# Optimization experiments

Measured on AMD Instinct MI355X. Metric: run time of the kernel, lower is better.

The kernel has to match this reference:

```python
import jax, jax.numpy as jnp
import numpy as np

B, DIM, H, W = 8, 256, 128, 128
P = 4               # patch_size
HEADS = 8
HD = DIM // HEADS   # head dim = 32
CPB_HIDDEN = 512    # hidden width of the dynamic RPE MLP


def setup_inputs() -> dict:
    key = jax.random.key(0)
    ks = jax.random.split(key, 12)
    s = 0.02
    return {
        "x": jax.random.normal(ks[0], (B, DIM, H, W), dtype=jnp.float32),
        # PatchEmbed2d: Conv2d(dim, dim, kernel=P, stride=P)  weight [O, I, P, P]
        "w_embed": jax.random.normal(ks[1], (DIM, DIM, P, P), dtype=jnp.float32) * s,
        "b_embed": jnp.zeros((DIM,), dtype=jnp.float32),
        # DynamicPosEncoder: MLP(2 -> CPB_HIDDEN -> HEADS) on relative coords
        "cpb_w1": jax.random.normal(ks[2], (CPB_HIDDEN, 2), dtype=jnp.float32) * s,
        "cpb_b1": jnp.zeros((CPB_HIDDEN,), dtype=jnp.float32),
        "cpb_w2": jax.random.normal(ks[3], (HEADS, CPB_HIDDEN), dtype=jnp.float32) * s,
        # MaskAttention2d
        "w_qkv": jax.random.normal(ks[4], (3 * DIM, DIM), dtype=jnp.float32) * s,
        "b_qkv": jnp.zeros((3 * DIM,), dtype=jnp.float32),
        "w_proj": jax.random.normal(ks[5], (DIM, DIM), dtype=jnp.float32) * s,
        "b_proj": jnp.zeros((DIM,), dtype=jnp.float32),
        # PatchUnEmbed2d: ConvTranspose2d(dim, dim, kernel=P, stride=P)  weight [I, O, P, P]
        "w_unembed": jax.random.normal(ks[6], (DIM, DIM, P, P), dtype=jnp.float32) * s,
        "b_unembed": jnp.zeros((DIM,), dtype=jnp.float32),
    }


def _rpe_bias(Hp, Wp, cpb_w1, cpb_b1, cpb_w2):
    """Dynamic relative position bias -> [HEADS, N, N], N = Hp*Wp."""
    # continuous relative-coordinate table [(2Hp-1)*(2Wp-1), 2], normalized to [-1, 1]
    rh = (jnp.arange(2 * Hp - 1, dtype=jnp.float32) - (Hp - 1)) / max(Hp - 1, 1)
    rw = (jnp.arange(2 * Wp - 1, dtype=jnp.float32) - (Wp - 1)) / max(Wp - 1, 1)
    rel = jnp.stack(jnp.meshgrid(rh, rw, indexing="ij"), axis=-1).reshape(-1, 2)
    table = jax.nn.relu(rel @ cpb_w1.T + cpb_b1) @ cpb_w2.T  # [(2Hp-1)(2Wp-1), HEADS]
    # static relative position index [N, N]
    ch = np.arange(Hp)
    cw = np.arange(Wp)
    coords = np.stack(np.meshgrid(ch, cw, indexing="ij")).reshape(2, -1)  # [2, N]
    d = coords[:, :, None] - coords[:, None, :]                           # [2, N, N]
    idx = (d[0] + Hp - 1) * (2 * Wp - 1) + (d[1] + Wp - 1)               # [N, N]
    bias = table[jnp.asarray(idx)]                                        # [N, N, HEADS]
    return bias.transpose(2, 0, 1)                                        # [HEADS, N, N]


def reference(x, w_embed, b_embed, cpb_w1, cpb_b1, cpb_w2,
              w_qkv, b_qkv, w_proj, b_proj, w_unembed, b_unembed):
    Bx, C, Hf, Wf = x.shape
    Hp, Wp = Hf // P, Wf // P
    N = Hp * Wp
    # ---- patch embed: Conv2d(k=P, s=P) as block reshape + einsum ----
    xr = x.reshape(Bx, C, Hp, P, Wp, P)
    z = jnp.einsum("bchpwq,ocpq->bohw", xr, w_embed) + b_embed[None, :, None, None]
    # ---- dynamic RPE bias ----
    bias = _rpe_bias(Hp, Wp, cpb_w1, cpb_b1, cpb_w2)  # [HEADS, N, N]
    # ---- multi-head self-attention over the Hp*Wp grid ----
    tok = z.reshape(Bx, C, N).transpose(0, 2, 1)                     # [B, N, C]
    qkv = tok @ w_qkv.T + b_qkv                                       # [B, N, 3C]
    qkv = qkv.reshape(Bx, N, 3, HEADS, HD).transpose(2, 0, 3, 1, 4)   # [3, B, H, N, hd]
    q, k, v = qkv[0], qkv[1], qkv[2]
    scale = HD ** -0.5
    attn = jnp.einsum("bhnd,bhmd->bhnm", q * scale, k) + bias[None]   # [B, H, N, N]
    attn = jax.nn.softmax(attn, axis=-1)
    out = jnp.einsum("bhnm,bhmd->bhnd", attn, v)                      # [B, H, N, hd]
    out = out.transpose(0, 2, 1, 3).reshape(Bx, N, C)
    out = out @ w_proj.T + b_proj                                     # [B, N, C]
    z2 = out.transpose(0, 2, 1).reshape(Bx, C, Hp, Wp)
    # ---- patch unembed: ConvTranspose2d(k=P, s=P) as einsum + block reshape ----
    y = jnp.einsum("bchw,copq->bohpwq", z2, w_unembed)
    y = y.reshape(Bx, C, Hf, Wf) + b_unembed[None, :, None, None]
    return y
```

## Files before the change

### kernel.cpp

```cpp
#include <hip/hip_runtime.h>
#include <cstdint>
#include <cstddef>


typedef __bf16 bf16x8 __attribute__((ext_vector_type(8)));
typedef float f32x4 __attribute__((ext_vector_type(4)));
typedef unsigned short u16x4 __attribute__((ext_vector_type(4)));

__device__ __forceinline__ unsigned short f2bf(float f) {
  unsigned u = __builtin_bit_cast(unsigned, f);
  u += 0x7fffu + ((u >> 16) & 1u);
  return (unsigned short)(u >> 16);
}
__device__ __forceinline__ float bf2f(unsigned short u) {
  return __builtin_bit_cast(float, ((unsigned)u) << 16);
}

__device__ __forceinline__ void async_ld16(const void* g, void* l) {
  __builtin_amdgcn_global_load_lds(
      (const __attribute__((address_space(1))) void*)g,
      (__attribute__((address_space(3))) void*)l, 16, 0, 0);
}

__global__ __launch_bounds__(256) void rpe_table_kernel(
    const float* __restrict__ w1, const float* __restrict__ b1,
    const float* __restrict__ w2, float* __restrict__ table) {
  int t = blockIdx.x * 256 + threadIdx.x;
  if (t >= 3969) return;
  int a = t / 63, c = t - a * 63;
  float rh = (float)(a - 31) * (1.0f / 31.0f);
  float rw = (float)(c - 31) * (1.0f / 31.0f);
  float acc[8];
#pragma unroll
  for (int h = 0; h < 8; h++) acc[h] = 0.f;
  for (int j = 0; j < 512; j++) {
    float hv = fmaxf(rh * w1[2 * j] + rw * w1[2 * j + 1] + b1[j], 0.f);
#pragma unroll
    for (int h = 0; h < 8; h++) acc[h] += hv * w2[h * 512 + j];
  }
#pragma unroll
  for (int h = 0; h < 8; h++) table[t * 8 + h] = acc[h];
}

__global__ __launch_bounds__(256) void bias_expand_kernel(
    const float* __restrict__ table, unsigned short* __restrict__ biasQK) {
  int t = blockIdx.x * 256 + threadIdx.x;
  int k8 = t & 127;
  int q = (t >> 7) & 1023;
  int h = t >> 17;
  int k0 = k8 * 8;
  int qh = q >> 5, qw = q & 31;
  int kh = k0 >> 5, kw0 = k0 & 31;
  int idxbase = (qh - kh + 31) * 63 + (qw - kw0 + 31);
  unsigned short pk[8];
#pragma unroll
  for (int j = 0; j < 8; j++)
    pk[j] = f2bf(table[(size_t)(idxbase - j) * 8 + h]);
  *(uint4*)(biasQK + ((size_t)h << 20) + (size_t)q * 1024 + k0) =
      *(const uint4*)pk;
}

__global__ __launch_bounds__(256) void cvt_bf16_kernel(
    const float* __restrict__ src, unsigned short* __restrict__ dst, int n8) {
  int i = blockIdx.x * 256 + threadIdx.x;
  if (i >= n8) return;
  const float4* s4 = (const float4*)src + (size_t)i * 2;
  float4 a = s4[0], b = s4[1];
  unsigned short t[8] = {f2bf(a.x), f2bf(a.y), f2bf(a.z), f2bf(a.w),
                         f2bf(b.x), f2bf(b.y), f2bf(b.z), f2bf(b.w)};
  *(uint4*)(dst + (size_t)i * 8) = *(const uint4*)t;
}

__global__ __launch_bounds__(256) void transpose_cvt_kernel(
    const float* __restrict__ src, unsigned short* __restrict__ dst) {
  __shared__ float tile[32][33];
  int bx = blockIdx.x;
  int by = blockIdx.y;
  int tx = threadIdx.x & 31, ty = threadIdx.x >> 5;
#pragma unroll
  for (int r = 0; r < 32; r += 8)
    tile[ty + r][tx] = src[(size_t)(by * 32 + ty + r) * 4096 + bx * 32 + tx];
  __syncthreads();
#pragma unroll
  for (int r = 0; r < 32; r += 8)
    dst[(size_t)(bx * 32 + ty + r) * 256 + by * 32 + tx] = f2bf(tile[tx][ty + r]);
}

__global__ __launch_bounds__(256) void im2col_bf16_kernel(
    const float* __restrict__ x, unsigned short* __restrict__ A) {
  int gid = blockIdx.x * 256 + threadIdx.x;
  int bn = gid & 8191;
  int c = gid >> 13;
  int b = bn >> 10;
  int hw = bn & 1023;
  int h = hw >> 5, w = hw & 31;
  const float4* x4 = (const float4*)x;
  int base = ((b * 256 + c) * 128 + 4 * h) * 32 + w;
  unsigned short t[16];
#pragma unroll
  for (int p = 0; p < 4; p++) {
    float4 v = x4[base + p * 32];
    t[p * 4 + 0] = f2bf(v.x); t[p * 4 + 1] = f2bf(v.y);
    t[p * 4 + 2] = f2bf(v.z); t[p * 4 + 3] = f2bf(v.w);
  }
  unsigned short* dst = A + (size_t)bn * 4096 + c * 16;
  *(uint4*)dst = *(const uint4*)t;
  *(uint4*)(dst + 8) = *(const uint4*)(t + 8);
}

__global__ __launch_bounds__(256) void splitk_reduce_kernel(
    const float* __restrict__ part, const float* __restrict__ bias,
    unsigned short* __restrict__ out) {
  size_t i = ((size_t)blockIdx.x * 256 + threadIdx.x) * 8;
  const float4* p = (const float4*)(part + i);
  const size_t s4 = 2097152 / 4;
  float4 a0 = p[0], a1 = p[1];
#pragma unroll
  for (int s = 1; s < 4; s++) {
    float4 b0 = p[s * s4], b1 = p[s * s4 + 1];
    a0.x += b0.x; a0.y += b0.y; a0.z += b0.z; a0.w += b0.w;
    a1.x += b1.x; a1.y += b1.y; a1.z += b1.z; a1.w += b1.w;
  }
  int col = (int)(i & 255);
  unsigned short t8[8] = {
      f2bf(a0.x + bias[col + 0]), f2bf(a0.y + bias[col + 1]),
      f2bf(a0.z + bias[col + 2]), f2bf(a0.w + bias[col + 3]),
      f2bf(a1.x + bias[col + 4]), f2bf(a1.y + bias[col + 5]),
      f2bf(a1.z + bias[col + 6]), f2bf(a1.w + bias[col + 7])};
  *(uint4*)(out + i) = *(const uint4*)t8;
}

template <int CMODE>
__global__ __launch_bounds__(256) void gemm_mfma_kernel(
    const unsigned short* __restrict__ A, const unsigned short* __restrict__ B,
    const float* __restrict__ bias, void* __restrict__ Cv,
    int M, int N, int K, int lda, int ldb, int ldc) {
  __shared__ unsigned short As[2 * 128 * 32];
  __shared__ unsigned short Bs[2 * 128 * 32];
  int tid = threadIdx.x;
  int lane = tid & 63;
  int wave = tid >> 6;
  int m0 = blockIdx.y * 128, n0 = blockIdx.x * 128;
  int wm = (wave & 1) * 64, wn = (wave >> 1) * 64;

  if (CMODE == 4) {
    int s = blockIdx.z;
    A += (size_t)s * K;
    B += (size_t)s * K;
    Cv = (void*)((float*)Cv + (size_t)s * M * N);
  }

  f32x4 acc[4][4];
#pragma unroll
  for (int i = 0; i < 4; i++)
#pragma unroll
    for (int j = 0; j < 4; j++) acc[i][j] = (f32x4){0.f, 0.f, 0.f, 0.f};

  int f0 = tid, f1 = tid + 256;
  const unsigned short* Ag0 = A + (size_t)(m0 + (f0 >> 2)) * lda + (f0 & 3) * 8;
  const unsigned short* Ag1 = A + (size_t)(m0 + (f1 >> 2)) * lda + (f1 & 3) * 8;
  const unsigned short* Bg0 = B + (size_t)(n0 + (f0 >> 2)) * ldb + (f0 & 3) * 8;
  const unsigned short* Bg1 = B + (size_t)(n0 + (f1 >> 2)) * ldb + (f1 & 3) * 8;
  unsigned short* Al0 = As + f0 * 8;
  unsigned short* Al1 = As + f1 * 8;
  unsigned short* Bl0 = Bs + f0 * 8;
  unsigned short* Bl1 = Bs + f1 * 8;

  int fr = lane & 15;
  int fh = lane >> 4;

  int ntiles = K >> 5;
  async_ld16(Ag0, Al0);
  async_ld16(Ag1, Al1);
  async_ld16(Bg0, Bl0);
  async_ld16(Bg1, Bl1);
  __syncthreads();

  for (int t = 0; t < ntiles; t++) {
    int cur = (t & 1) << 12;
    int nxt = cur ^ 4096;
    if (t + 1 < ntiles) {
      int kn = (t + 1) << 5;
      async_ld16(Ag0 + kn, Al0 + nxt);
      async_ld16(Ag1 + kn, Al1 + nxt);
      async_ld16(Bg0 + kn, Bl0 + nxt);
      async_ld16(Bg1 + kn, Bl1 + nxt);
    }
    const unsigned short* Asc = As + cur;
    const unsigned short* Bsc = Bs + cur;
    bf16x8 af[4], bfr[4];
#pragma unroll
    for (int tt = 0; tt < 4; tt++) {
      af[tt] = *(const bf16x8*)(Asc + (wm + tt * 16 + fr) * 32 + fh * 8);
      bfr[tt] = *(const bf16x8*)(Bsc + (wn + tt * 16 + fr) * 32 + fh * 8);
    }
#pragma unroll
    for (int mt = 0; mt < 4; mt++)
#pragma unroll
      for (int nt = 0; nt < 4; nt++)
        acc[mt][nt] = __builtin_amdgcn_mfma_f32_16x16x32_bf16(
            af[mt], bfr[nt], acc[mt][nt], 0, 0, 0);
    __syncthreads();
  }

#pragma unroll
  for (int mt = 0; mt < 4; mt++) {
    int row0 = m0 + wm + mt * 16 + fh * 4;
    if (CMODE == 2) {
      int b = row0 >> 10, hp = (row0 >> 5) & 31, wp = row0 & 31;
      size_t rowoff0 = (size_t)b * 4194304 + hp * 512 + wp * 4;
      float* y = (float*)Cv;
#pragma unroll
      for (int nt = 0; nt < 4; nt++) {
        int col = n0 + wn + nt * 16 + fr;
        int o = col >> 4, p = (col >> 2) & 3, q = col & 3;
        size_t coloff = (size_t)o * 16384 + p * 128 + q;
        float bv = bias[o];
#pragma unroll
        for (int r = 0; r < 4; r++)
          y[rowoff0 + r * 4 + coloff] = acc[mt][nt][r] + bv;
      }
    } else if (CMODE == 3) {
      unsigned short* base = (unsigned short*)Cv;
#pragma unroll
      for (int nt = 0; nt < 4; nt++) {
        int col = n0 + wn + nt * 16 + fr;
        int which = col >> 8, hh = (col >> 5) & 7, d = col & 31;
        float bv = bias[col];
#pragma unroll
        for (int r = 0; r < 4; r++) {
          int row = row0 + r;
          int bb = row >> 10, nn = row & 1023;
          int bh = bb * 8 + hh;
          float v = acc[mt][nt][r] + bv;
          if (which == 0) v *= 0.17677669529663687f;
          size_t addr;
          if (which < 2)
            addr = (size_t)which * 2097152 + ((size_t)bh * 1024 + nn) * 32 + d;
          else
            addr = (size_t)2 * 2097152 + (size_t)bh * 32768 + (size_t)d * 1024 + nn;
          base[addr] = f2bf(v);
        }
      }
    } else if (CMODE == 4) {
      float* Cp = (float*)Cv;
#pragma unroll
      for (int nt = 0; nt < 4; nt++) {
        int col = n0 + wn + nt * 16 + fr;
#pragma unroll
        for (int r = 0; r < 4; r++)
          Cp[(size_t)(row0 + r) * ldc + col] = acc[mt][nt][r];
      }
    } else {
#pragma unroll
      for (int nt = 0; nt < 4; nt++) {
        int col = n0 + wn + nt * 16 + fr;
        float bv = bias ? bias[col] : 0.f;
        unsigned short* C = (unsigned short*)Cv;
#pragma unroll
        for (int r = 0; r < 4; r++)
          C[(size_t)(row0 + r) * ldc + col] = f2bf(acc[mt][nt][r] + bv);
      }
    }
  }
}

__global__ __launch_bounds__(256) void attn_mfma_kernel(
    const unsigned short* __restrict__ Qb, const unsigned short* __restrict__ Kb,
    const unsigned short* __restrict__ Vtb,
    const unsigned short* __restrict__ biasQK,
    unsigned short* __restrict__ out) {
  __shared__ unsigned short sm[21888];
  unsigned short* Ks = sm;
  unsigned short* Vt = sm + 2304;
  unsigned short* Bsh = sm + 4480;
  unsigned short* Qs = sm + 13184;
  unsigned short* Ps = sm + 13184;

  int tid = threadIdx.x;
  int lane = tid & 63, w = tid >> 6;
  int n = lane & 15, g = lane >> 4;
  int blk = blockIdx.x;
  int qt = blk & 7, b = (blk >> 3) & 7, h = blk >> 6;
  int bh = b * 8 + h;
  int q0 = qt * 128;

  const unsigned short* Qg = Qb + ((size_t)bh * 1024 + q0) * 32;
  const unsigned short* Kg = Kb + (size_t)bh * 1024 * 32;
  const unsigned short* Vg = Vtb + (size_t)bh * 32 * 1024;
  const unsigned short* Bg = biasQK + ((size_t)h << 20) + (size_t)q0 * 1024;

#pragma unroll
  for (int i = 0; i < 2; i++) {
    int idx = i * 256 + tid;
    int r = idx >> 2, c = idx & 3;
    *(uint4*)(Qs + r * 36 + c * 8) = *(const uint4*)(Qg + (size_t)r * 32 + c * 8);
  }
  __syncthreads();
  bf16x8 qf[2];
  qf[0] = *(const bf16x8*)(Qs + (w * 32 + n) * 36 + g * 8);
  qf[1] = *(const bf16x8*)(Qs + (w * 32 + 16 + n) * 36 + g * 8);

  f32x4 oacc[2][2];
#pragma unroll
  for (int i = 0; i < 2; i++)
#pragma unroll
    for (int j = 0; j < 2; j++) oacc[i][j] = (f32x4){0.f, 0.f, 0.f, 0.f};
  float m_run[2] = {-1e30f, -1e30f}, l_run[2] = {0.f, 0.f};

  unsigned short* Pw = Ps + w * 2176;

  for (int ks = 0; ks < 16; ks++) {
    int k0 = ks * 64;
    __syncthreads();
    {
      int r = tid >> 2, c = tid & 3;
      *(uint4*)(Ks + r * 36 + c * 8) =
          *(const uint4*)(Kg + (size_t)(k0 + r) * 32 + c * 8);
    }
    {
      int d = tid >> 3, c = tid & 7;
      *(uint4*)(Vt + d * 68 + c * 8) =
          *(const uint4*)(Vg + (size_t)d * 1024 + k0 + c * 8);
    }
#pragma unroll
    for (int i = 0; i < 4; i++) {
      int idx = i * 256 + tid;
      int r = idx >> 3, c = idx & 7;
      *(uint4*)(Bsh + r * 68 + c * 8) =
          *(const uint4*)(Bg + (size_t)r * 1024 + k0 + c * 8);
    }
    __syncthreads();

    bf16x8 kf[4];
#pragma unroll
    for (int mt = 0; mt < 4; mt++)
      kf[mt] = *(const bf16x8*)(Ks + (mt * 16 + n) * 36 + g * 8);
    f32x4 s[4][2];
#pragma unroll
    for (int mt = 0; mt < 4; mt++)
#pragma unroll
      for (int nt = 0; nt < 2; nt++)
        s[mt][nt] = __builtin_amdgcn_mfma_f32_16x16x32_bf16(
            kf[mt], qf[nt], (f32x4){0.f, 0.f, 0.f, 0.f}, 0, 0, 0);

#pragma unroll
    for (int mt = 0; mt < 4; mt++)
#pragma unroll
      for (int nt = 0; nt < 2; nt++) {
        u16x4 bb = *(const u16x4*)(Bsh + (w * 32 + nt * 16 + n) * 68 +
                                   mt * 16 + g * 4);
#pragma unroll
        for (int r = 0; r < 4; r++) s[mt][nt][r] += bf2f(bb[r]);
      }

    float alpha[2];
#pragma unroll
    for (int nt = 0; nt < 2; nt++) {
      float mx = -1e30f;
#pragma unroll
      for (int mt = 0; mt < 4; mt++)
#pragma unroll
        for (int r = 0; r < 4; r++) mx = fmaxf(mx, s[mt][nt][r]);
      mx = fmaxf(mx, __shfl_xor(mx, 16, 64));
      mx = fmaxf(mx, __shfl_xor(mx, 32, 64));
      float m_new = fmaxf(m_run[nt], mx);
      alpha[nt] = __expf(m_run[nt] - m_new);
      m_run[nt] = m_new;
      float ls = 0.f;
#pragma unroll
      for (int mt = 0; mt < 4; mt++) {
#pragma unroll
        for (int r = 0; r < 4; r++) {
          float p = __expf(s[mt][nt][r] - m_new);
          s[mt][nt][r] = p;
          ls += p;
        }
        u16x4 pk = {f2bf(s[mt][nt][0]), f2bf(s[mt][nt][1]),
                    f2bf(s[mt][nt][2]), f2bf(s[mt][nt][3])};
        *(u16x4*)(Pw + (nt * 16 + n) * 68 + mt * 16 + g * 4) = pk;
      }
      ls += __shfl_xor(ls, 16, 64);
      ls += __shfl_xor(ls, 32, 64);
      l_run[nt] = l_run[nt] * alpha[nt] + ls;
    }

#pragma unroll
    for (int dt = 0; dt < 2; dt++)
#pragma unroll
      for (int nt = 0; nt < 2; nt++)
#pragma unroll
        for (int r = 0; r < 4; r++) oacc[dt][nt][r] *= alpha[nt];
#pragma unroll
    for (int kt = 0; kt < 2; kt++) {
      bf16x8 vf[2], pf[2];
#pragma unroll
      for (int dt = 0; dt < 2; dt++)
        vf[dt] = *(const bf16x8*)(Vt + (dt * 16 + n) * 68 + kt * 32 + g * 8);
#pragma unroll
      for (int nt = 0; nt < 2; nt++)
        pf[nt] = *(const bf16x8*)(Pw + (nt * 16 + n) * 68 + kt * 32 + g * 8);
#pragma unroll
      for (int dt = 0; dt < 2; dt++)
#pragma unroll
        for (int nt = 0; nt < 2; nt++)
          oacc[dt][nt] = __builtin_amdgcn_mfma_f32_16x16x32_bf16(
              vf[dt], pf[nt], oacc[dt][nt], 0, 0, 0);
    }
  }

  float inv[2] = {1.f / l_run[0], 1.f / l_run[1]};
#pragma unroll
  for (int dt = 0; dt < 2; dt++)
#pragma unroll
    for (int nt = 0; nt < 2; nt++)
#pragma unroll
      for (int r = 0; r < 4; r++) {
        int d = dt * 16 + g * 4 + r;
        int q = q0 + w * 32 + nt * 16 + n;
        out[(size_t)(b * 1024 + q) * 256 + h * 32 + d] =
            f2bf(oacc[dt][nt][r] * inv[nt]);
      }
}

extern "C" void kernel_launch(void* const* d_in, const int* in_sizes, int n_in,
                              void* d_out, int out_size, void* d_ws, size_t ws_size,
                              hipStream_t stream) {
  const float* x         = (const float*)d_in[0];
  const float* w_embed   = (const float*)d_in[1];
  const float* b_embed   = (const float*)d_in[2];
  const float* cpb_w1    = (const float*)d_in[3];
  const float* cpb_b1    = (const float*)d_in[4];
  const float* cpb_w2    = (const float*)d_in[5];
  const float* w_qkv     = (const float*)d_in[6];
  const float* b_qkv     = (const float*)d_in[7];
  const float* w_proj    = (const float*)d_in[8];
  const float* b_proj    = (const float*)d_in[9];
  const float* w_unembed = (const float*)d_in[10];
  const float* b_unembed = (const float*)d_in[11];
  float* out = (float*)d_out;

  char* w = (char*)d_ws;
  unsigned short* Abig  = (unsigned short*)w; w += (size_t)8192 * 4096 * 2;
  unsigned short* tok   = (unsigned short*)w; w += (size_t)8192 * 256 * 2;
  unsigned short* qkvB  = (unsigned short*)w; w += (size_t)3 * 2097152 * 2;
  unsigned short* attno = (unsigned short*)w; w += (size_t)8192 * 256 * 2;
  unsigned short* z2    = (unsigned short*)w; w += (size_t)8192 * 256 * 2;
  float*          table = (float*)w;          w += (size_t)32768 * 4;
  unsigned short* biasQ = (unsigned short*)w; w += (size_t)8388608 * 2;
  unsigned short* wE    = (unsigned short*)w; w += (size_t)1048576 * 2;
  unsigned short* wQ    = (unsigned short*)w; w += (size_t)196608 * 2;
  unsigned short* wP    = (unsigned short*)w; w += (size_t)65536 * 2;
  unsigned short* wUt   = (unsigned short*)w; w += (size_t)1048576 * 2;

  unsigned short* Qb  = qkvB;
  unsigned short* Kb  = qkvB + 2097152;
  unsigned short* Vtb = qkvB + 2 * 2097152;

  float* Cpart = (float*)qkvB;

  cvt_bf16_kernel<<<512, 256, 0, stream>>>(w_embed, wE, 131072);
  cvt_bf16_kernel<<<96, 256, 0, stream>>>(w_qkv, wQ, 24576);
  cvt_bf16_kernel<<<32, 256, 0, stream>>>(w_proj, wP, 8192);
  transpose_cvt_kernel<<<dim3(128, 8), 256, 0, stream>>>(w_unembed, wUt);
  im2col_bf16_kernel<<<8192, 256, 0, stream>>>(x, Abig);

  gemm_mfma_kernel<4><<<dim3(2, 64, 4), 256, 0, stream>>>(
      Abig, wE, nullptr, Cpart, 8192, 256, 1024, 4096, 4096, 256);
  splitk_reduce_kernel<<<1024, 256, 0, stream>>>(Cpart, b_embed, tok);

  rpe_table_kernel<<<16, 256, 0, stream>>>(cpb_w1, cpb_b1, cpb_w2, table);
  bias_expand_kernel<<<4096, 256, 0, stream>>>(table, biasQ);

  gemm_mfma_kernel<3><<<dim3(6, 64), 256, 0, stream>>>(
      tok, wQ, b_qkv, qkvB, 8192, 768, 256, 256, 256, 0);
  attn_mfma_kernel<<<512, 256, 0, stream>>>(Qb, Kb, Vtb, biasQ, attno);
  gemm_mfma_kernel<1><<<dim3(2, 64), 256, 0, stream>>>(
      attno, wP, b_proj, z2, 8192, 256, 256, 256, 256, 256);
  gemm_mfma_kernel<2><<<dim3(32, 64), 256, 0, stream>>>(
      z2, wUt, b_unembed, out, 8192, 4096, 256, 256, 256, 0);
}
```

Measured before the change: 562.0 us.

## Compute RPE bias on the fly from LDS table, double-buffer K/V in attention

```diff
diff --git a/kernel.cpp b/kernel.cpp
--- a/kernel.cpp
+++ b/kernel.cpp
@@ -24,7 +24,7 @@
 
 __global__ __launch_bounds__(256) void rpe_table_kernel(
     const float* __restrict__ w1, const float* __restrict__ b1,
-    const float* __restrict__ w2, float* __restrict__ table) {
+    const float* __restrict__ w2, float* __restrict__ tableT) {
   int t = blockIdx.x * 256 + threadIdx.x;
   if (t >= 3969) return;
   int a = t / 63, c = t - a * 63;
@@ -39,25 +39,7 @@
     for (int h = 0; h < 8; h++) acc[h] += hv * w2[h * 512 + j];
   }
 #pragma unroll
-  for (int h = 0; h < 8; h++) table[t * 8 + h] = acc[h];
-}
-
-__global__ __launch_bounds__(256) void bias_expand_kernel(
-    const float* __restrict__ table, unsigned short* __restrict__ biasQK) {
-  int t = blockIdx.x * 256 + threadIdx.x;
-  int k8 = t & 127;
-  int q = (t >> 7) & 1023;
-  int h = t >> 17;
-  int k0 = k8 * 8;
-  int qh = q >> 5, qw = q & 31;
-  int kh = k0 >> 5, kw0 = k0 & 31;
-  int idxbase = (qh - kh + 31) * 63 + (qw - kw0 + 31);
-  unsigned short pk[8];
-#pragma unroll
-  for (int j = 0; j < 8; j++)
-    pk[j] = f2bf(table[(size_t)(idxbase - j) * 8 + h]);
-  *(uint4*)(biasQK + ((size_t)h << 20) + (size_t)q * 1024 + k0) =
-      *(const uint4*)pk;
+  for (int h = 0; h < 8; h++) tableT[h * 4096 + t] = acc[h];
 }
 
 __global__ __launch_bounds__(256) void cvt_bf16_kernel(
@@ -265,17 +247,17 @@
   }
 }
 
-__global__ __launch_bounds__(256) void attn_mfma_kernel(
+__global__ __launch_bounds__(512) void attn_mfma_kernel(
     const unsigned short* __restrict__ Qb, const unsigned short* __restrict__ Kb,
     const unsigned short* __restrict__ Vtb,
-    const unsigned short* __restrict__ biasQK,
+    const float* __restrict__ tableT,
     unsigned short* __restrict__ out) {
-  __shared__ unsigned short sm[21888];
-  unsigned short* Ks = sm;
-  unsigned short* Vt = sm + 2304;
-  unsigned short* Bsh = sm + 4480;
-  unsigned short* Qs = sm + 13184;
-  unsigned short* Ps = sm + 13184;
+  __shared__ float smf[12804];
+  float* th = smf;
+  unsigned short* Ks = (unsigned short*)(smf + 3972);
+  unsigned short* Vt = (unsigned short*)(smf + 6276);
+  unsigned short* Ps = (unsigned short*)(smf + 8452);
+  unsigned short* Qs = (unsigned short*)(smf + 8452);
 
   int tid = threadIdx.x;
   int lane = tid & 63, w = tid >> 6;
@@ -288,139 +270,125 @@
   const unsigned short* Qg = Qb + ((size_t)bh * 1024 + q0) * 32;
   const unsigned short* Kg = Kb + (size_t)bh * 1024 * 32;
   const unsigned short* Vg = Vtb + (size_t)bh * 32 * 1024;
-  const unsigned short* Bg = biasQK + ((size_t)h << 20) + (size_t)q0 * 1024;
-
-#pragma unroll
-  for (int i = 0; i < 2; i++) {
-    int idx = i * 256 + tid;
-    int r = idx >> 2, c = idx & 3;
+  const float* tg = tableT + (size_t)h * 4096;
+
+  {
+    int r = tid >> 2, c = tid & 3;
     *(uint4*)(Qs + r * 36 + c * 8) = *(const uint4*)(Qg + (size_t)r * 32 + c * 8);
   }
+  for (int i = tid; i < 3969; i += 512) th[i] = tg[i];
+
+  bool isK = tid < 256;
+  int cidx = isK ? tid : tid - 256;
+  const unsigned short* gsrc = isK
+      ? (Kg + (size_t)(cidx >> 2) * 32 + (cidx & 3) * 8)
+      : (Vg + (size_t)(cidx >> 3) * 1024 + (cidx & 7) * 8);
+  int gstep = isK ? 2048 : 64;
+  unsigned short* lbase = isK ? Ks : Vt;
+  int loff = isK ? ((cidx >> 2) * 36 + (cidx & 3) * 8)
+                 : ((cidx >> 3) * 68 + (cidx & 7) * 8);
+  int lbufstep = isK ? 2304 : 2176;
+
+  uint4 greg = *(const uint4*)(gsrc);
   __syncthreads();
-  bf16x8 qf[2];
-  qf[0] = *(const bf16x8*)(Qs + (w * 32 + n) * 36 + g * 8);
-  qf[1] = *(const bf16x8*)(Qs + (w * 32 + 16 + n) * 36 + g * 8);
-
-  f32x4 oacc[2][2];
-#pragma unroll
-  for (int i = 0; i < 2; i++)
-#pragma unroll
-    for (int j = 0; j < 2; j++) oacc[i][j] = (f32x4){0.f, 0.f, 0.f, 0.f};
-  float m_run[2] = {-1e30f, -1e30f}, l_run[2] = {0.f, 0.f};
-
-  unsigned short* Pw = Ps + w * 2176;
-
-  for (int ks = 0; ks < 16; ks++) {
-    int k0 = ks * 64;
+
+  bf16x8 qf = *(const bf16x8*)(Qs + (w * 16 + n) * 36 + g * 8);
+
+  *(uint4*)(lbase + loff) = greg;
+  greg = *(const uint4*)(gsrc + gstep);
+  __syncthreads();
+
+  f32x4 oacc[2];
+#pragma unroll
+  for (int i = 0; i < 2; i++) oacc[i] = (f32x4){0.f, 0.f, 0.f, 0.f};
+  float m_run = -1e30f, l_run = 0.f;
+
+  unsigned short* Pw = Ps + w * 1088;
+  int q = q0 + w * 16 + n;
+  int qh = q >> 5, qw = q & 31;
+
+  for (int t = 0; t < 16; t++) {
+    const unsigned short* Kc = Ks + (t & 1) * 2304;
+    const unsigned short* Vc = Vt + (t & 1) * 2176;
+    int k0 = t * 64;
+
+    f32x4 s[4];
+    __builtin_amdgcn_s_setprio(1);
+#pragma unroll
+    for (int mt = 0; mt < 4; mt++) {
+      bf16x8 kf = *(const bf16x8*)(Kc + (mt * 16 + n) * 36 + g * 8);
+      s[mt] = __builtin_amdgcn_mfma_f32_16x16x32_bf16(
+          kf, qf, (f32x4){0.f, 0.f, 0.f, 0.f}, 0, 0, 0);
+    }
+    __builtin_amdgcn_s_setprio(0);
+
+#pragma unroll
+    for (int mt = 0; mt < 4; mt++) {
+      int kb = k0 + mt * 16 + g * 4;
+      int ib = (qh - (kb >> 5) + 31) * 63 + (qw - (kb & 31) + 31);
+      s[mt][0] += th[ib];
+      s[mt][1] += th[ib - 1];
+      s[mt][2] += th[ib - 2];
+      s[mt][3] += th[ib - 3];
+    }
+
+    float mx = -1e30f;
+#pragma unroll
+    for (int mt = 0; mt < 4; mt++)
+#pragma unroll
+      for (int r = 0; r < 4; r++) mx = fmaxf(mx, s[mt][r]);
+    mx = fmaxf(mx, __shfl_xor(mx, 16, 64));
+    mx = fmaxf(mx, __shfl_xor(mx, 32, 64));
+    float m_new = fmaxf(m_run, mx);
+    float alpha = __expf(m_run - m_new);
+    m_run = m_new;
+    float ls = 0.f;
+#pragma unroll
+    for (int mt = 0; mt < 4; mt++) {
+#pragma unroll
+      for (int r = 0; r < 4; r++) {
+        float p = __expf(s[mt][r] - m_new);
+        s[mt][r] = p;
+        ls += p;
+      }
+      u16x4 pk = {f2bf(s[mt][0]), f2bf(s[mt][1]), f2bf(s[mt][2]),
+                  f2bf(s[mt][3])};
+      *(u16x4*)(Pw + n * 68 + mt * 16 + g * 4) = pk;
+    }
+    ls += __shfl_xor(ls, 16, 64);
+    ls += __shfl_xor(ls, 32, 64);
+    l_run = l_run * alpha + ls;
+
+#pragma unroll
+    for (int dt = 0; dt < 2; dt++)
+#pragma unroll
+      for (int r = 0; r < 4; r++) oacc[dt][r] *= alpha;
+    __builtin_amdgcn_s_setprio(1);
+#pragma unroll
+    for (int kt = 0; kt < 2; kt++) {
+      bf16x8 vf0 = *(const bf16x8*)(Vc + n * 68 + kt * 32 + g * 8);
+      bf16x8 vf1 = *(const bf16x8*)(Vc + (16 + n) * 68 + kt * 32 + g * 8);
+      bf16x8 pf = *(const bf16x8*)(Pw + n * 68 + kt * 32 + g * 8);
+      oacc[0] = __builtin_amdgcn_mfma_f32_16x16x32_bf16(vf0, pf, oacc[0], 0, 0, 0);
+      oacc[1] = __builtin_amdgcn_mfma_f32_16x16x32_bf16(vf1, pf, oacc[1], 0, 0, 0);
+    }
+    __builtin_amdgcn_s_setprio(0);
+
+    if (t < 15) {
+      *(uint4*)(lbase + ((t + 1) & 1) * lbufstep + loff) = greg;
+      if (t < 14) greg = *(const uint4*)(gsrc + (size_t)(t + 2) * gstep);
+    }
     __syncthreads();
-    {
-      int r = tid >> 2, c = tid & 3;
-      *(uint4*)(Ks + r * 36 + c * 8) =
-          *(const uint4*)(Kg + (size_t)(k0 + r) * 32 + c * 8);
-    }
-    {
-      int d = tid >> 3, c = tid & 7;
-      *(uint4*)(Vt + d * 68 + c * 8) =
-          *(const uint4*)(Vg + (size_t)d * 1024 + k0 + c * 8);
-    }
-#pragma unroll
-    for (int i = 0; i < 4; i++) {
-      int idx = i * 256 + tid;
-      int r = idx >> 3, c = idx & 7;
-      *(uint4*)(Bsh + r * 68 + c * 8) =
-          *(const uint4*)(Bg + (size_t)r * 1024 + k0 + c * 8);
-    }
-    __syncthreads();
-
-    bf16x8 kf[4];
-#pragma unroll
-    for (int mt = 0; mt < 4; mt++)
-      kf[mt] = *(const bf16x8*)(Ks + (mt * 16 + n) * 36 + g * 8);
-    f32x4 s[4][2];
-#pragma unroll
-    for (int mt = 0; mt < 4; mt++)
-#pragma unroll
-      for (int nt = 0; nt < 2; nt++)
-        s[mt][nt] = __builtin_amdgcn_mfma_f32_16x16x32_bf16(
-            kf[mt], qf[nt], (f32x4){0.f, 0.f, 0.f, 0.f}, 0, 0, 0);
-
-#pragma unroll
-    for (int mt = 0; mt < 4; mt++)
-#pragma unroll
-      for (int nt = 0; nt < 2; nt++) {
-        u16x4 bb = *(const u16x4*)(Bsh + (w * 32 + nt * 16 + n) * 68 +
-                                   mt * 16 + g * 4);
-#pragma unroll
-        for (int r = 0; r < 4; r++) s[mt][nt][r] += bf2f(bb[r]);
-      }
-
-    float alpha[2];
-#pragma unroll
-    for (int nt = 0; nt < 2; nt++) {
-      float mx = -1e30f;
-#pragma unroll
-      for (int mt = 0; mt < 4; mt++)
-#pragma unroll
-        for (int r = 0; r < 4; r++) mx = fmaxf(mx, s[mt][nt][r]);
-      mx = fmaxf(mx, __shfl_xor(mx, 16, 64));
-      mx = fmaxf(mx, __shfl_xor(mx, 32, 64));
-      float m_new = fmaxf(m_run[nt], mx);
-      alpha[nt] = __expf(m_run[nt] - m_new);
-      m_run[nt] = m_new;
-      float ls = 0.f;
-#pragma unroll
-      for (int mt = 0; mt < 4; mt++) {
-#pragma unroll
-        for (int r = 0; r < 4; r++) {
-          float p = __expf(s[mt][nt][r] - m_new);
-          s[mt][nt][r] = p;
-          ls += p;
-        }
-        u16x4 pk = {f2bf(s[mt][nt][0]), f2bf(s[mt][nt][1]),
-                    f2bf(s[mt][nt][2]), f2bf(s[mt][nt][3])};
-        *(u16x4*)(Pw + (nt * 16 + n) * 68 + mt * 16 + g * 4) = pk;
-      }
-      ls += __shfl_xor(ls, 16, 64);
-      ls += __shfl_xor(ls, 32, 64);
-      l_run[nt] = l_run[nt] * alpha[nt] + ls;
-    }
-
-#pragma unroll
-    for (int dt = 0; dt < 2; dt++)
-#pragma unroll
-      for (int nt = 0; nt < 2; nt++)
-#pragma unroll
-        for (int r = 0; r < 4; r++) oacc[dt][nt][r] *= alpha[nt];
-#pragma unroll
-    for (int kt = 0; kt < 2; kt++) {
-      bf16x8 vf[2], pf[2];
-#pragma unroll
-      for (int dt = 0; dt < 2; dt++)
-        vf[dt] = *(const bf16x8*)(Vt + (dt * 16 + n) * 68 + kt * 32 + g * 8);
-#pragma unroll
-      for (int nt = 0; nt < 2; nt++)
-        pf[nt] = *(const bf16x8*)(Pw + (nt * 16 + n) * 68 + kt * 32 + g * 8);
-#pragma unroll
-      for (int dt = 0; dt < 2; dt++)
-#pragma unroll
-        for (int nt = 0; nt < 2; nt++)
-          oacc[dt][nt] = __builtin_amdgcn_mfma_f32_16x16x32_bf16(
-              vf[dt], pf[nt], oacc[dt][nt], 0, 0, 0);
-    }
-  }
-
-  float inv[2] = {1.f / l_run[0], 1.f / l_run[1]};
-#pragma unroll
-  for (int dt = 0; dt < 2; dt++)
-#pragma unroll
-    for (int nt = 0; nt < 2; nt++)
-#pragma unroll
-      for (int r = 0; r < 4; r++) {
-        int d = dt * 16 + g * 4 + r;
-        int q = q0 + w * 32 + nt * 16 + n;
-        out[(size_t)(b * 1024 + q) * 256 + h * 32 + d] =
-            f2bf(oacc[dt][nt][r] * inv[nt]);
-      }
+  }
+
+  float invl = 1.f / l_run;
+  unsigned short* ob = out + ((size_t)(b * 1024 + q) * 256) + h * 32;
+#pragma unroll
+  for (int dt = 0; dt < 2; dt++) {
+    u16x4 o4 = {f2bf(oacc[dt][0] * invl), f2bf(oacc[dt][1] * invl),
+                f2bf(oacc[dt][2] * invl), f2bf(oacc[dt][3] * invl)};
+    *(u16x4*)(ob + dt * 16 + g * 4) = o4;
+  }
 }
 
 extern "C" void kernel_launch(void* const* d_in, const int* in_sizes, int n_in,
@@ -443,40 +411,40 @@
   char* w = (char*)d_ws;
   unsigned short* Abig  = (unsigned short*)w; w += (size_t)8192 * 4096 * 2;
   unsigned short* tok   = (unsigned short*)w; w += (size_t)8192 * 256 * 2;
-  unsigned short* qkvB  = (unsigned short*)w; w += (size_t)3 * 2097152 * 2;
-  unsigned short* attno = (unsigned short*)w; w += (size_t)8192 * 256 * 2;
-  unsigned short* z2    = (unsigned short*)w; w += (size_t)8192 * 256 * 2;
-  float*          table = (float*)w;          w += (size_t)32768 * 4;
-  unsigned short* biasQ = (unsigned short*)w; w += (size_t)8388608 * 2;
   unsigned short* wE    = (unsigned short*)w; w += (size_t)1048576 * 2;
   unsigned short* wQ    = (unsigned short*)w; w += (size_t)196608 * 2;
   unsigned short* wP    = (unsigned short*)w; w += (size_t)65536 * 2;
   unsigned short* wUt   = (unsigned short*)w; w += (size_t)1048576 * 2;
-
+  float*          tableT= (float*)w;          w += (size_t)32768 * 4;
+  float*          PART  = (float*)w;          w += (size_t)8388608 * 4;
+
+  unsigned short* qkvB  = (unsigned short*)PART;
+  unsigned short* attno = (unsigned short*)((char*)PART + 12582912);
+  unsigned short* z2    = (unsigned short*)((char*)PART + 16777216);
   unsigned short* Qb  = qkvB;
   unsigned short* Kb  = qkvB + 2097152;
   unsigned short* Vtb = qkvB + 2 * 2097152;
-
-  float* Cpart = (float*)qkvB;
 
   cvt_bf16_kernel<<<512, 256, 0, stream>>>(w_embed, wE, 131072);
   cvt_bf16_kernel<<<96, 256, 0, stream>>>(w_qkv, wQ, 24576);
   cvt_bf16_kernel<<<32, 256, 0, stream>>>(w_proj, wP, 8192);
   transpose_cvt_kernel<<<dim3(128, 8), 256, 0, stream>>>(w_unembed, wUt);
   im2col_bf16_kernel<<<8192, 256, 0, stream>>>(x, Abig);
+  rpe_table_kernel<<<16, 256, 0, stream>>>(cpb_w1, cpb_b1, cpb_w2, tableT);
 
   gemm_mfma_kernel<4><<<dim3(2, 64, 4), 256, 0, stream>>>(
-      Abig, wE, nullptr, Cpart, 8192, 256, 1024, 4096, 4096, 256);
-  splitk_reduce_kernel<<<1024, 256, 0, stream>>>(Cpart, b_embed, tok);
-
-  rpe_table_kernel<<<16, 256, 0, stream>>>(cpb_w1, cpb_b1, cpb_w2, table);
-  bias_expand_kernel<<<4096, 256, 0, stream>>>(table, biasQ);
+      Abig, wE, nullptr, PART, 8192, 256, 1024, 4096, 4096, 256);
+  splitk_reduce_kernel<<<1024, 256, 0, stream>>>(PART, b_embed, tok);
 
   gemm_mfma_kernel<3><<<dim3(6, 64), 256, 0, stream>>>(
       tok, wQ, b_qkv, qkvB, 8192, 768, 256, 256, 256, 0);
-  attn_mfma_kernel<<<512, 256, 0, stream>>>(Qb, Kb, Vtb, biasQ, attno);
-  gemm_mfma_kernel<1><<<dim3(2, 64), 256, 0, stream>>>(
-      attno, wP, b_proj, z2, 8192, 256, 256, 256, 256, 256);
+
+  attn_mfma_kernel<<<512, 512, 0, stream>>>(Qb, Kb, Vtb, tableT, attno);
+
+  gemm_mfma_kernel<4><<<dim3(2, 64, 4), 256, 0, stream>>>(
+      attno, wP, nullptr, (float*)Abig, 8192, 256, 64, 256, 256, 256);
+  splitk_reduce_kernel<<<1024, 256, 0, stream>>>((float*)Abig, b_proj, z2);
+
   gemm_mfma_kernel<2><<<dim3(32, 64), 256, 0, stream>>>(
       z2, wUt, b_unembed, out, 8192, 4096, 256, 256, 256, 0);
 }
```

After: 562.4 us. Within noise of the previous version (+0.1%).
